# Kernel optimization log

Hardware: AMD Instinct MI355X
Metric: run time of the kernel (lower is better)

The kernel has to match this reference:

```python
import jax, jax.numpy as jnp
import numpy as np
from jax import lax

N_BOXES = 6000
IOU_THR = 0.5
CONF_THR = 0.6


def setup_inputs() -> dict:
    key = jax.random.key(0)
    k1, k2, k3 = jax.random.split(key, 3)
    # valid xyxy boxes: top-left in [0,1000), width/height in [1,101)
    xy = jax.random.uniform(k1, (N_BOXES, 2), dtype=jnp.float32) * 1000.0
    wh = jax.random.uniform(k2, (N_BOXES, 2), dtype=jnp.float32) * 100.0 + 1.0
    boxes = jnp.concatenate([xy, xy + wh], axis=-1)  # [N,4] x1,y1,x2,y2
    scores = jax.random.uniform(k3, (N_BOXES,), dtype=jnp.float32)
    return {"boxes": boxes, "scores": scores}


def _pairwise_iou(b):
    # b: [N,4] xyxy. Returns [N,N] IoU, coordinates handled separately to
    # avoid materializing [N,N,2] intermediates.
    x1, y1, x2, y2 = b[:, 0], b[:, 1], b[:, 2], b[:, 3]
    area = (x2 - x1) * (y2 - y1)  # [N]
    iw = jnp.clip(jnp.minimum(x2[:, None], x2[None, :]) - jnp.maximum(x1[:, None], x1[None, :]), 0.0)
    ih = jnp.clip(jnp.minimum(y2[:, None], y2[None, :]) - jnp.maximum(y1[:, None], y1[None, :]), 0.0)
    inter = iw * ih  # [N,N]
    return inter / (area[:, None] + area[None, :] - inter)


def reference(boxes, scores):
    """torchvision-style NMS (suppress IoU > 0.5) then confidence filter (>= 0.6).
    Returns masked scores [N]: score where the box survives both stages, else 0.
    (Fixed-shape mask form of the original index outputs, for jit compatibility.)
    """
    n = scores.shape[0]
    order = jnp.argsort(-scores)  # descending by confidence
    iou = _pairwise_iou(boxes[order])  # [N,N] in sorted order
    idx = jnp.arange(n)

    def body(suppressed, i):
        keep_i = jnp.logical_not(suppressed[i])
        # a kept box suppresses all lower-scoring boxes with IoU > threshold
        supp_new = keep_i & (iou[i] > IOU_THR) & (idx > i)
        return suppressed | supp_new, keep_i

    _, keep_sorted = lax.scan(body, jnp.zeros((n,), dtype=bool), idx)
    keep = jnp.zeros((n,), dtype=bool).at[order].set(keep_sorted)
    final = keep & (scores >= CONF_THR)
    return jnp.where(final, scores, 0.0)
```

## Files before the change

kernel.cpp:

```cpp
#include <hip/hip_runtime.h>
#include <stdint.h>

#define N_BOXES 6000
#define NT 94
#define NTP 96
#define NROWS (NTP * 64)
#define CAP 16
#define IOU_THR 0.5f
#define CONF_THR 0.6f

typedef unsigned long long u64;
typedef unsigned int u32;
typedef unsigned short u16;

#define BAR() asm volatile("s_waitcnt lgkmcnt(0)\n\ts_barrier" ::: "memory")

__device__ __forceinline__ u64 rdlane64(u64 v, int l) {
    unsigned lo = (unsigned)__builtin_amdgcn_readlane((int)(unsigned)v, l);
    unsigned hi = (unsigned)__builtin_amdgcn_readlane((int)(unsigned)(v >> 32), l);
    return ((u64)hi << 32) | lo;
}

__global__ void __launch_bounds__(1024) k_sort(const float* __restrict__ scores,
                                               const float4* __restrict__ boxes,
                                               int* __restrict__ sidx,
                                               float4* __restrict__ sboxes,
                                               u32* __restrict__ lists_w,
                                               int* __restrict__ cnt) {
    __shared__ u64 kt[N_BOXES];
    __shared__ int part[1024];
    const int tid = threadIdx.x;
    const int gtid = blockIdx.x * 1024 + tid;
    for (int j = gtid; j < NROWS * CAP / 2; j += NT * 1024) lists_w[j] = 0xFFFFFFFFu;
    for (int j = gtid; j < NROWS; j += NT * 1024) cnt[j] = 0;

    for (int j = tid; j < N_BOXES; j += 1024) {
        unsigned inv = ~__float_as_uint(scores[j]);
        kt[j] = ((u64)inv << 32) | (unsigned)j;
    }
    __syncthreads();
    const int il = tid & 63;
    const int i = blockIdx.x * 64 + il;
    const int j0 = (tid >> 6) * 375;
    u64 mykey = (i < N_BOXES) ? kt[i] : 0ull;
    int cntr = 0;
#pragma unroll 5
    for (int jj = 0; jj < 375; ++jj)
        cntr += (kt[j0 + jj] < mykey) ? 1 : 0;
    part[tid] = cntr;
    __syncthreads();
    if (tid < 64 && i < N_BOXES) {
        int r = 0;
#pragma unroll
        for (int s = 0; s < 16; ++s) r += part[il + 64 * s];
        sidx[r] = i;
        sboxes[r] = boxes[i];
    }
}

__global__ void k_mask(const float4* __restrict__ sboxes,
                       u16* __restrict__ lists, int* __restrict__ cnt,
                       u64* __restrict__ diagw) {
    int ct = blockIdx.x, rt = blockIdx.y;
    if (ct < rt) return;
    int lane = threadIdx.x;
    __shared__ float4 rb[64];
    int row0 = rt * 64;
    int rows = min(64, N_BOXES - row0);
    if (lane < rows) rb[lane] = sboxes[row0 + lane];
    __syncthreads();
    int j = ct * 64 + lane;
    bool jvalid = (j < N_BOXES);
    float4 cb = make_float4(0.f, 0.f, 1.f, 1.f);
    if (jvalid) cb = sboxes[j];
    float carea = (cb.z - cb.x) * (cb.w - cb.y);
    bool isdiag = (ct == rt);
    for (int i = 0; i < rows; ++i) {
        float4 rbx = rb[i];
        float rarea = (rbx.z - rbx.x) * (rbx.w - rbx.y);
        float iw = fmaxf(fminf(rbx.z, cb.z) - fmaxf(rbx.x, cb.x), 0.f);
        float ih = fmaxf(fminf(rbx.w, cb.w) - fmaxf(rbx.y, cb.y), 0.f);
        float inter = iw * ih;
        float iou = inter / ((rarea + carea) - inter);
        int row = row0 + i;
        bool pred = jvalid && (j > row) && (iou > IOU_THR);
        if (isdiag) {
            u64 bal = __ballot(pred);
            if (lane == (i & 63)) diagw[row] = bal;
        } else if (pred) {
            int slot = atomicAdd(&cnt[row], 1);
            if (slot < CAP) lists[row * CAP + slot] = (u16)j;
        }
    }
}

__global__ void __launch_bounds__(256) k_scan(const u16* __restrict__ lists,
                                              const u64* __restrict__ diagw,
                                              const int* __restrict__ sidx,
                                              const float* __restrict__ scores,
                                              float* __restrict__ out) {
    __shared__ u64 removed[NTP];
    __shared__ u64 kwbuf[NTP];
    const int tid   = threadIdx.x;
    const int lane  = tid & 63;
    const int row_l = tid >> 2;
    const int sg    = (tid & 3) * 4;
    if (tid < NTP) removed[tid] = 0;

    u64 L0, L1, L2, D0, D1, D2;
    L0 = *(const u64*)&lists[(0 * 64 + row_l) * CAP + sg];
    L1 = *(const u64*)&lists[(1 * 64 + row_l) * CAP + sg];
    L2 = *(const u64*)&lists[(2 * 64 + row_l) * CAP + sg];
    D0 = diagw[0 * 64 + lane];
    D1 = diagw[1 * 64 + lane];
    D2 = diagw[2 * 64 + lane];
    __syncthreads();

#define STEP(T, LUSE, DUSE)                                                    \
    {                                                                          \
        const u64 nz = __ballot(DUSE != 0ull);        \
        const int row0 = (T) * 64;                                             \
        const int rem = N_BOXES - row0;                                        \
        const u64 valid = (rem >= 64) ? ~0ull                                  \
                        : ((rem <= 0) ? 0ull : ((1ull << rem) - 1ull));        \
        u64 c = valid & ~removed[(T)];                                         \
        u64 kw = 0;                                                            \
        while (c) {                                                            \
            u64 blockers = c & nz;                                             \
            if (!blockers) { kw |= c; break; }             \
            int g = (int)__builtin_ctzll(blockers);                            \
            u64 below = c & ((1ull << g) - 1ull);         \
            kw |= below | (1ull << g);                                         \
            u64 df = rdlane64(DUSE, g);                     \
            c &= ~(df | below | (1ull << g));                                  \
        }                                                                      \
        if (tid == 0) kwbuf[(T)] = kw;                                         \
        if (((kw >> row_l) & 1ull) && LUSE != ~0ull) {                         \
            u16 e0 = (u16)(LUSE), e1 = (u16)(LUSE >> 16),                      \
                e2 = (u16)(LUSE >> 32), e3 = (u16)(LUSE >> 48);                \
            if (e0 != 0xFFFFu) atomicOr(&removed[e0 >> 6], 1ull << (e0 & 63)); \
            if (e1 != 0xFFFFu) atomicOr(&removed[e1 >> 6], 1ull << (e1 & 63)); \
            if (e2 != 0xFFFFu) atomicOr(&removed[e2 >> 6], 1ull << (e2 & 63)); \
            if (e3 != 0xFFFFu) atomicOr(&removed[e3 >> 6], 1ull << (e3 & 63)); \
        }                                                                      \
        const int tn = ((T) + 3 < NTP) ? ((T) + 3) : ((T) + 3 - NTP);          \
        LUSE = *(const u64*)&lists[(tn * 64 + row_l) * CAP + sg];              \
        DUSE = diagw[tn * 64 + lane];                                          \
        BAR();                                                                 \
    }

    for (int t = 0; t < NTP; t += 3) {
        STEP(t,     L0, D0)
        STEP(t + 1, L1, D1)
        STEP(t + 2, L2, D2)
    }
#undef STEP

    for (int p = tid; p < N_BOXES; p += 256) {
        int orig = sidx[p];
        float s = scores[orig];
        bool k = (kwbuf[p >> 6] >> (p & 63)) & 1ull;
        out[orig] = (k && (s >= CONF_THR)) ? s : 0.0f;
    }
}

extern "C" void kernel_launch(void* const* d_in, const int* in_sizes, int n_in,
                              void* d_out, int out_size, void* d_ws, size_t ws_size,
                              hipStream_t stream) {
    const float* boxes  = (const float*)d_in[0];
    const float* scores = (const float*)d_in[1];
    float* out = (float*)d_out;

    char* ws = (char*)d_ws;
    u16*    lists  = (u16*)(ws);
    int*    cnt    = (int*)(ws + 196608);
    u64*    diagw  = (u64*)(ws + 221184);
    int*    sidx   = (int*)(ws + 270336);
    float4* sboxes = (float4*)(ws + 294336);

    k_sort<<<dim3(NT), dim3(1024), 0, stream>>>(scores, (const float4*)boxes, sidx,
                                                sboxes, (u32*)lists, cnt);
    k_mask<<<dim3(NT, NT), dim3(64), 0, stream>>>((const float4*)sboxes, lists, cnt, diagw);
    k_scan<<<dim3(1), dim3(256), 0, stream>>>(lists, diagw, sidx, scores, out);
}
```

Measured before the change: 132.8 us.

## Run serial NMS scan in a single wavefront without block barriers, warm cache with other waves

The sequential tile scan now runs entirely in wave 0, with each lane handling a whole 16-entry suppression list. That removes the per-tile block-wide barrier, and the removed bitmask for the next tile is read after the wave's own LDS atomics. The other three waves stream the lists and diagonal buffers once and XOR the values into a dummy accumulator, which pulls them into cache for the latency-bound wave. The trade-off is more serial atomics per lane and reliance on in-wave ordering of LDS operations.

```diff
diff --git a/kernel.cpp b/kernel.cpp
--- a/kernel.cpp
+++ b/kernel.cpp
@@ -12,8 +12,6 @@
 typedef unsigned long long u64;
 typedef unsigned int u32;
 typedef unsigned short u16;
-
-#define BAR() asm volatile("s_waitcnt lgkmcnt(0)\n\ts_barrier" ::: "memory")
 
 __device__ __forceinline__ u64 rdlane64(u64 v, int l) {
     unsigned lo = (unsigned)__builtin_amdgcn_readlane((int)(unsigned)v, l);
@@ -101,60 +99,84 @@
                                               float* __restrict__ out) {
     __shared__ u64 removed[NTP];
     __shared__ u64 kwbuf[NTP];
-    const int tid   = threadIdx.x;
-    const int lane  = tid & 63;
-    const int row_l = tid >> 2;
-    const int sg    = (tid & 3) * 4;
+    const int tid = threadIdx.x;
     if (tid < NTP) removed[tid] = 0;
-
-    u64 L0, L1, L2, D0, D1, D2;
-    L0 = *(const u64*)&lists[(0 * 64 + row_l) * CAP + sg];
-    L1 = *(const u64*)&lists[(1 * 64 + row_l) * CAP + sg];
-    L2 = *(const u64*)&lists[(2 * 64 + row_l) * CAP + sg];
-    D0 = diagw[0 * 64 + lane];
-    D1 = diagw[1 * 64 + lane];
-    D2 = diagw[2 * 64 + lane];
-    __syncthreads();
-
-#define STEP(T, LUSE, DUSE)                                                    \
-    {                                                                          \
-        const u64 nz = __ballot(DUSE != 0ull);        \
-        const int row0 = (T) * 64;                                             \
-        const int rem = N_BOXES - row0;                                        \
-        const u64 valid = (rem >= 64) ? ~0ull                                  \
-                        : ((rem <= 0) ? 0ull : ((1ull << rem) - 1ull));        \
-        u64 c = valid & ~removed[(T)];                                         \
-        u64 kw = 0;                                                            \
-        while (c) {                                                            \
-            u64 blockers = c & nz;                                             \
-            if (!blockers) { kw |= c; break; }             \
-            int g = (int)__builtin_ctzll(blockers);                            \
-            u64 below = c & ((1ull << g) - 1ull);         \
-            kw |= below | (1ull << g);                                         \
-            u64 df = rdlane64(DUSE, g);                     \
-            c &= ~(df | below | (1ull << g));                                  \
-        }                                                                      \
-        if (tid == 0) kwbuf[(T)] = kw;                                         \
-        if (((kw >> row_l) & 1ull) && LUSE != ~0ull) {                         \
-            u16 e0 = (u16)(LUSE), e1 = (u16)(LUSE >> 16),                      \
-                e2 = (u16)(LUSE >> 32), e3 = (u16)(LUSE >> 48);                \
-            if (e0 != 0xFFFFu) atomicOr(&removed[e0 >> 6], 1ull << (e0 & 63)); \
+    __syncthreads();
+
+    if (tid >= 64) {
+        const uint4* lv = (const uint4*)lists;
+        const uint4* dv = (const uint4*)diagw;
+        u32 acc = 0;
+        for (int j = tid - 64; j < 12288; j += 192) {
+            uint4 v = lv[j];
+            acc ^= v.x ^ v.y ^ v.z ^ v.w;
+        }
+        for (int j = tid - 64; j < 3072; j += 192) {
+            uint4 v = dv[j];
+            acc ^= v.x ^ v.y ^ v.z ^ v.w;
+        }
+        asm volatile("" :: "v"(acc));
+    } else {
+        const int lane = tid;
+        uint4 A0 = *(const uint4*)&lists[(0 * 64 + lane) * CAP];
+        uint4 B0 = *(const uint4*)&lists[(0 * 64 + lane) * CAP + 8];
+        uint4 A1 = *(const uint4*)&lists[(1 * 64 + lane) * CAP];
+        uint4 B1 = *(const uint4*)&lists[(1 * 64 + lane) * CAP + 8];
+        uint4 A2 = *(const uint4*)&lists[(2 * 64 + lane) * CAP];
+        uint4 B2 = *(const uint4*)&lists[(2 * 64 + lane) * CAP + 8];
+        u64 D0 = diagw[0 * 64 + lane];
+        u64 D1 = diagw[1 * 64 + lane];
+        u64 D2 = diagw[2 * 64 + lane];
+        u64 rmn = 0;
+
+#define SC2(w)                                                                 \
+        if ((w) != 0xFFFFFFFFu) {                                              \
+            u16 e0 = (u16)(w), e1 = (u16)((w) >> 16);                          \
+            atomicOr(&removed[e0 >> 6], 1ull << (e0 & 63));                    \
             if (e1 != 0xFFFFu) atomicOr(&removed[e1 >> 6], 1ull << (e1 & 63)); \
-            if (e2 != 0xFFFFu) atomicOr(&removed[e2 >> 6], 1ull << (e2 & 63)); \
-            if (e3 != 0xFFFFu) atomicOr(&removed[e3 >> 6], 1ull << (e3 & 63)); \
-        }                                                                      \
-        const int tn = ((T) + 3 < NTP) ? ((T) + 3) : ((T) + 3 - NTP);          \
-        LUSE = *(const u64*)&lists[(tn * 64 + row_l) * CAP + sg];              \
-        DUSE = diagw[tn * 64 + lane];                                          \
-        BAR();                                                                 \
-    }
-
-    for (int t = 0; t < NTP; t += 3) {
-        STEP(t,     L0, D0)
-        STEP(t + 1, L1, D1)
-        STEP(t + 2, L2, D2)
-    }
+        }
+
+#define STEP(T, A, B, DD)                                                      \
+        {                                                                      \
+            const u64 nz = __ballot(DD != 0ull);      \
+            const int row0 = (T) * 64;                                         \
+            const int rem = N_BOXES - row0;                                    \
+            const u64 valid = (rem >= 64) ? ~0ull                              \
+                            : ((rem <= 0) ? 0ull : ((1ull << rem) - 1ull));    \
+            u64 c = valid & ~rmn;                                              \
+            u64 kw = 0;                                                        \
+            while (c) {                                                        \
+                u64 blockers = c & nz;                                         \
+                if (!blockers) { kw |= c; break; }         \
+                int g = (int)__builtin_ctzll(blockers);                        \
+                u64 below = c & ((1ull << g) - 1ull);     \
+                kw |= below | (1ull << g);                                     \
+                u64 df = rdlane64(DD, g);                   \
+                c &= ~(df | below | (1ull << g));                              \
+            }                                                                  \
+            if (((kw >> lane) & 1ull) && A.x != 0xFFFFFFFFu) {                 \
+                SC2(A.x) SC2(A.y) SC2(A.z) SC2(A.w)                            \
+                SC2(B.x) SC2(B.y) SC2(B.z) SC2(B.w)                            \
+            }                                                                  \
+              \
+               \
+            rmn = removed[((T) + 1 < NTP) ? (T) + 1 : 0];                      \
+            if (lane == 0) kwbuf[(T)] = kw;                                    \
+            const int tn = ((T) + 3 < NTP) ? ((T) + 3) : ((T) + 3 - NTP);      \
+            A = *(const uint4*)&lists[(tn * 64 + lane) * CAP];                 \
+            B = *(const uint4*)&lists[(tn * 64 + lane) * CAP + 8];             \
+            DD = diagw[tn * 64 + lane];                                        \
+        }
+
+        for (int t = 0; t < NTP; t += 3) {
+            STEP(t,     A0, B0, D0)
+            STEP(t + 1, A1, B1, D1)
+            STEP(t + 2, A2, B2, D2)
+        }
 #undef STEP
+#undef SC2
+    }
+    __syncthreads();
 
     for (int p = tid; p < N_BOXES; p += 256) {
         int orig = sidx[p];
```

After: 140.9 us. 6.1% more time.

## Use ballot-based rank sort and triangular grid for IoU mask kernel

Applied to the files above, without the earlier changes.

The rank sort no longer stages keys in shared memory with per-thread serial comparisons. Each wave now ranks four boxes by streaming all scores from global memory and counting smaller keys with ballot plus popcount. The mask kernel launches only the upper-triangular tile blocks, mapped from a linear block index, instead of a full square grid where half the blocks exit early. This cuts empty block launches and shared-memory sort overhead, at the cost of repeated global score reads per wave and a sqrt-based index decode.

```diff
diff --git a/kernel.cpp b/kernel.cpp
--- a/kernel.cpp
+++ b/kernel.cpp
@@ -6,6 +6,7 @@
 #define NTP 96
 #define NROWS (NTP * 64)
 #define CAP 16
+#define NCHUNK 94
 #define IOU_THR 0.5f
 #define CONF_THR 0.6f
 
@@ -27,42 +28,55 @@
                                                float4* __restrict__ sboxes,
                                                u32* __restrict__ lists_w,
                                                int* __restrict__ cnt) {
-    __shared__ u64 kt[N_BOXES];
-    __shared__ int part[1024];
     const int tid = threadIdx.x;
     const int gtid = blockIdx.x * 1024 + tid;
     for (int j = gtid; j < NROWS * CAP / 2; j += NT * 1024) lists_w[j] = 0xFFFFFFFFu;
     for (int j = gtid; j < NROWS; j += NT * 1024) cnt[j] = 0;
 
-    for (int j = tid; j < N_BOXES; j += 1024) {
-        unsigned inv = ~__float_as_uint(scores[j]);
-        kt[j] = ((u64)inv << 32) | (unsigned)j;
-    }
-    __syncthreads();
-    const int il = tid & 63;
-    const int i = blockIdx.x * 64 + il;
-    const int j0 = (tid >> 6) * 375;
-    u64 mykey = (i < N_BOXES) ? kt[i] : 0ull;
-    int cntr = 0;
-#pragma unroll 5
-    for (int jj = 0; jj < 375; ++jj)
-        cntr += (kt[j0 + jj] < mykey) ? 1 : 0;
-    part[tid] = cntr;
-    __syncthreads();
-    if (tid < 64 && i < N_BOXES) {
-        int r = 0;
+    const int w = tid >> 6;
+    const int lane = tid & 63;
+    u64 own[4];
+    int ob[4];
 #pragma unroll
-        for (int s = 0; s < 16; ++s) r += part[il + 64 * s];
-        sidx[r] = i;
-        sboxes[r] = boxes[i];
+    for (int q = 0; q < 4; ++q) {
+        ob[q] = blockIdx.x * 64 + w * 4 + q;
+        float s = (ob[q] < N_BOXES) ? scores[ob[q]] : 0.0f;
+        own[q] = ((u64)(~__float_as_uint(s)) << 32) | (unsigned)ob[q];
+    }
+    int rank0 = 0, rank1 = 0, rank2 = 0, rank3 = 0;
+#pragma unroll 2
+    for (int cb = 0; cb < NCHUNK; ++cb) {
+        int j = cb * 64 + lane;
+        u64 kk = ~0ull;
+        if (j < N_BOXES) {
+            unsigned inv = ~__float_as_uint(scores[j]);
+            kk = ((u64)inv << 32) | (unsigned)j;
+        }
+        rank0 += __popcll(__ballot(kk < own[0]));
+        rank1 += __popcll(__ballot(kk < own[1]));
+        rank2 += __popcll(__ballot(kk < own[2]));
+        rank3 += __popcll(__ballot(kk < own[3]));
+    }
+    if (lane == 0) {
+        int r[4] = {rank0, rank1, rank2, rank3};
+#pragma unroll
+        for (int q = 0; q < 4; ++q)
+            if (ob[q] < N_BOXES) {
+                sidx[r[q]] = ob[q];
+                sboxes[r[q]] = boxes[ob[q]];
+            }
     }
 }
 
 __global__ void k_mask(const float4* __restrict__ sboxes,
                        u16* __restrict__ lists, int* __restrict__ cnt,
                        u64* __restrict__ diagw) {
-    int ct = blockIdx.x, rt = blockIdx.y;
-    if (ct < rt) return;
+    const int b = blockIdx.x;
+    int v = (int)((sqrtf(8.0f * (float)b + 1.0f) - 1.0f) * 0.5f);
+    while ((v + 1) * (v + 2) / 2 <= b) ++v;
+    while (v * (v + 1) / 2 > b) --v;
+    const int rt = b - v * (v + 1) / 2;
+    const int ct = v;
     int lane = threadIdx.x;
     __shared__ float4 rb[64];
     int row0 = rt * 64;
@@ -180,6 +194,7 @@
 
     k_sort<<<dim3(NT), dim3(1024), 0, stream>>>(scores, (const float4*)boxes, sidx,
                                                 sboxes, (u32*)lists, cnt);
-    k_mask<<<dim3(NT, NT), dim3(64), 0, stream>>>((const float4*)sboxes, lists, cnt, diagw);
+    k_mask<<<dim3(NT * (NT + 1) / 2), dim3(64), 0, stream>>>((const float4*)sboxes,
+                                                             lists, cnt, diagw);
     k_scan<<<dim3(1), dim3(256), 0, stream>>>(lists, diagw, sidx, scores, out);
 }
```

Result: slower. 145.4 us (+9.4%).

## Fuse sort, mask and scan into one cooperative kernel with per-row-tile readiness flags

Applied to the files above, without the earlier changes.

Replaces the three launches with a single cooperative kernel. NT blocks sort, then after a grid sync compute the IoU mask over a flattened list of upper-triangle tile pairs. One extra block runs the sequential NMS scan, polling per-row-tile done counters so it can start on early tiles while the mask is still being computed. List entries switch to a zero-initialised, flag-bit encoding written with atomicOr so the scanner can read partially filled lists with atomic loads. This removes launch gaps and overlaps the serial scan with the mask work, at the cost of a grid sync, spin polling, and a fallback path if the cooperative launch fails.

```diff
diff --git a/kernel.cpp b/kernel.cpp
--- a/kernel.cpp
+++ b/kernel.cpp
@@ -1,11 +1,16 @@
 #include <hip/hip_runtime.h>
+#include <hip/hip_cooperative_groups.h>
 #include <stdint.h>
+
+namespace cg = cooperative_groups;
 
 #define N_BOXES 6000
 #define NT 94
 #define NTP 96
 #define NROWS (NTP * 64)
 #define CAP 16
+#define NPAIRS (NT * (NT + 1) / 2)
+#define NWAVES (NT * 16)
 #define IOU_THR 0.5f
 #define CONF_THR 0.6f
 
@@ -19,6 +24,192 @@
     unsigned lo = (unsigned)__builtin_amdgcn_readlane((int)(unsigned)v, l);
     unsigned hi = (unsigned)__builtin_amdgcn_readlane((int)(unsigned)(v >> 32), l);
     return ((u64)hi << 32) | lo;
+}
+
+__global__ void __launch_bounds__(1024) k_fused(
+        const float* __restrict__ scores, const float4* __restrict__ boxes,
+        int* __restrict__ sidx, float4* __restrict__ sboxes,
+        u16* __restrict__ lists, int* __restrict__ cnt,
+        u64* __restrict__ diagw, int* __restrict__ done,
+        float* __restrict__ out) {
+    __shared__ __align__(16) char shraw[52096];
+    u64*    kt      = (u64*)shraw;
+    int*    part    = (int*)(shraw + 48000);
+    float4* rb      = (float4*)shraw;
+    u64*    removed = (u64*)shraw;
+    u64*    kwbuf   = (u64*)(shraw + 768);
+
+    const int tid  = threadIdx.x;
+    const int bid  = blockIdx.x;
+    const int w    = tid >> 6;
+    const int lane = tid & 63;
+
+    if (bid < NT) {
+        const int gtid = bid * 1024 + tid;
+        u32* lists_w = (u32*)lists;
+        for (int j = gtid; j < NROWS * CAP / 2; j += NT * 1024) lists_w[j] = 0u;
+        for (int j = gtid; j < NROWS; j += NT * 1024) cnt[j] = 0;
+        for (int j = tid; j < N_BOXES; j += 1024) {
+            unsigned inv = ~__float_as_uint(scores[j]);
+            kt[j] = ((u64)inv << 32) | (unsigned)j;
+        }
+        __syncthreads();
+        const int i = bid * 64 + lane;
+        const int j0 = w * 375;
+        u64 mykey = (i < N_BOXES) ? kt[i] : 0ull;
+        int cntr = 0;
+#pragma unroll 5
+        for (int jj = 0; jj < 375; ++jj)
+            cntr += (kt[j0 + jj] < mykey) ? 1 : 0;
+        part[tid] = cntr;
+        __syncthreads();
+        if (tid < 64 && i < N_BOXES) {
+            int r = 0;
+#pragma unroll
+            for (int s = 0; s < 16; ++s) r += part[lane + 64 * s];
+            sidx[r] = i;
+            sboxes[r] = boxes[i];
+        }
+    } else {
+        if (tid < NTP) done[tid] = 0;
+    }
+    cg::this_grid().sync();
+
+    if (bid < NT) {
+        const int gw = bid * 16 + w;
+        u32* lw = (u32*)lists;
+        for (int p = gw; p < NPAIRS; p += NWAVES) {
+            int rt = (int)((189.0f - sqrtf(35721.0f - 8.0f * (float)p)) * 0.5f);
+            while ((189 * rt - rt * rt) / 2 > p) --rt;
+            while ((189 * (rt + 1) - (rt + 1) * (rt + 1)) / 2 <= p) ++rt;
+            const int ct = rt + (p - (189 * rt - rt * rt) / 2);
+            const int row0 = rt * 64;
+            const int rows = min(64, N_BOXES - row0);
+            if (lane < rows) rb[w * 64 + lane] = sboxes[row0 + lane];
+            const int j = ct * 64 + lane;
+            const bool jvalid = (j < N_BOXES);
+            float4 cb = make_float4(0.f, 0.f, 1.f, 1.f);
+            if (jvalid) cb = sboxes[j];
+            float carea = (cb.z - cb.x) * (cb.w - cb.y);
+            const bool isdiag = (ct == rt);
+            for (int i = 0; i < rows; ++i) {
+                float4 rbx = rb[w * 64 + i];
+                float rarea = (rbx.z - rbx.x) * (rbx.w - rbx.y);
+                float iw = fmaxf(fminf(rbx.z, cb.z) - fmaxf(rbx.x, cb.x), 0.f);
+                float ih = fmaxf(fminf(rbx.w, cb.w) - fmaxf(rbx.y, cb.y), 0.f);
+                float inter = iw * ih;
+                float iou = inter / ((rarea + carea) - inter);
+                int row = row0 + i;
+                bool pred = jvalid && (j > row) && (iou > IOU_THR);
+                if (isdiag) {
+                    u64 bal = __ballot(pred);
+                    if (lane == (i & 63))
+                        __hip_atomic_store(&diagw[row], bal, __ATOMIC_RELAXED,
+                                           __HIP_MEMORY_SCOPE_AGENT);
+                } else if (pred) {
+                    int slot = atomicAdd(&cnt[row], 1);
+                    if (slot < CAP) {
+                        int e = row * CAP + slot;
+                        u32 val = ((u32)j | 0x8000u) << ((e & 1) * 16);
+                        atomicOr(&lw[e >> 1], val);
+                    }
+                }
+            }
+            asm volatile("s_waitcnt vmcnt(0)" ::: "memory");
+            if (lane == 0)
+                __hip_atomic_fetch_add(&done[rt], 1, __ATOMIC_RELAXED,
+                                       __HIP_MEMORY_SCOPE_AGENT);
+        }
+        return;
+    }
+
+#define POLL()                                                                 \
+    {                                                                          \
+        bool r0_ = (__hip_atomic_load(&done[lane], __ATOMIC_RELAXED,           \
+                        __HIP_MEMORY_SCOPE_AGENT) == NT - lane);               \
+        int t1_ = 64 + lane;                                                   \
+        bool r1_ = (t1_ >= NT) || (__hip_atomic_load(&done[t1_],               \
+                        __ATOMIC_RELAXED, __HIP_MEMORY_SCOPE_AGENT)            \
+                        == NT - t1_);                                          \
+        u64 nb0_ = ~__ballot(r0_);                                             \
+        u64 nb1_ = ~__ballot(r1_);                                             \
+        rdy = nb0_ ? (int)__builtin_ctzll(nb0_)                                \
+                   : (nb1_ ? 64 + (int)__builtin_ctzll(nb1_) : 128);           \
+    }
+#define WAITR(need)                                                            \
+    while (rdy < (need)) { POLL(); if (rdy < (need)) __builtin_amdgcn_s_sleep(2); }
+#define ALD(p) __hip_atomic_load((u64*)(p), __ATOMIC_RELAXED, __HIP_MEMORY_SCOPE_AGENT)
+
+    if (tid < 256) {
+        const int row_l = tid >> 2;
+        const int sg    = (tid & 3) * 4;
+        if (tid < NTP) removed[tid] = 0;
+        int rdy = 0;
+        WAITR(3);
+        u64 L0, L1, L2, D0, D1, D2;
+        L0 = ALD(&lists[(0 * 64 + row_l) * CAP + sg]);
+        L1 = ALD(&lists[(1 * 64 + row_l) * CAP + sg]);
+        L2 = ALD(&lists[(2 * 64 + row_l) * CAP + sg]);
+        D0 = ALD(&diagw[0 * 64 + lane]);
+        D1 = ALD(&diagw[1 * 64 + lane]);
+        D2 = ALD(&diagw[2 * 64 + lane]);
+        __syncthreads();
+
+#define FSTEP(T, LUSE, DUSE)                                                   \
+    {                                                                          \
+        const u64 nz = __ballot(DUSE != 0ull);                                 \
+        const int row0 = (T) * 64;                                             \
+        const int rem = N_BOXES - row0;                                        \
+        const u64 valid = (rem >= 64) ? ~0ull                                  \
+                        : ((rem <= 0) ? 0ull : ((1ull << rem) - 1ull));        \
+        u64 c = valid & ~removed[(T)];                                         \
+        u64 kw = 0;                                                            \
+        while (c) {                                                            \
+            u64 blockers = c & nz;                                             \
+            if (!blockers) { kw |= c; break; }                                 \
+            int g = (int)__builtin_ctzll(blockers);                            \
+            u64 below = c & ((1ull << g) - 1ull);                              \
+            kw |= below | (1ull << g);                                         \
+            u64 df = rdlane64(DUSE, g);                                        \
+            c &= ~(df | below | (1ull << g));                                  \
+        }                                                                      \
+        if (tid == 0) kwbuf[(T)] = kw;                                         \
+        if (((kw >> row_l) & 1ull) && LUSE != 0ull) {                          \
+            u32 e0 = (u32)(LUSE) & 0xFFFFu, e1 = (u32)(LUSE) >> 16;            \
+            u32 e2 = (u32)(LUSE >> 32) & 0xFFFFu, e3 = (u32)(LUSE >> 48);      \
+            if (e0 & 0x8000u) atomicOr(&removed[(e0 & 0x7FFFu) >> 6], 1ull << (e0 & 63)); \
+            if (e1 & 0x8000u) atomicOr(&removed[(e1 & 0x7FFFu) >> 6], 1ull << (e1 & 63)); \
+            if (e2 & 0x8000u) atomicOr(&removed[(e2 & 0x7FFFu) >> 6], 1ull << (e2 & 63)); \
+            if (e3 & 0x8000u) atomicOr(&removed[(e3 & 0x7FFFu) >> 6], 1ull << (e3 & 63)); \
+        }                                                                      \
+        const int tn = ((T) + 3 < NTP) ? ((T) + 3) : ((T) + 3 - NTP);          \
+        const int nd = (tn < NT) ? tn + 1 : 0;                                 \
+        WAITR(nd);                                                             \
+        LUSE = ALD(&lists[(tn * 64 + row_l) * CAP + sg]);                      \
+        DUSE = ALD(&diagw[tn * 64 + lane]);                                    \
+        BAR();                                                                 \
+    }
+
+        for (int t = 0; t < NTP; t += 3) {
+            FSTEP(t,     L0, D0)
+            FSTEP(t + 1, L1, D1)
+            FSTEP(t + 2, L2, D2)
+        }
+#undef FSTEP
+    } else {
+        __syncthreads();
+        for (int t = 0; t < NTP; ++t) BAR();
+    }
+
+    for (int p = tid; p < N_BOXES; p += 1024) {
+        int orig = sidx[p];
+        float s = scores[orig];
+        bool k = (kwbuf[p >> 6] >> (p & 63)) & 1ull;
+        out[orig] = (k && (s >= CONF_THR)) ? s : 0.0f;
+    }
+#undef POLL
+#undef WAITR
+#undef ALD
 }
 
 __global__ void __launch_bounds__(1024) k_sort(const float* __restrict__ scores,
@@ -33,7 +224,6 @@
     const int gtid = blockIdx.x * 1024 + tid;
     for (int j = gtid; j < NROWS * CAP / 2; j += NT * 1024) lists_w[j] = 0xFFFFFFFFu;
     for (int j = gtid; j < NROWS; j += NT * 1024) cnt[j] = 0;
-
     for (int j = tid; j < N_BOXES; j += 1024) {
         unsigned inv = ~__float_as_uint(scores[j]);
         kt[j] = ((u64)inv << 32) | (unsigned)j;
@@ -106,7 +296,6 @@
     const int row_l = tid >> 2;
     const int sg    = (tid & 3) * 4;
     if (tid < NTP) removed[tid] = 0;
-
     u64 L0, L1, L2, D0, D1, D2;
     L0 = *(const u64*)&lists[(0 * 64 + row_l) * CAP + sg];
     L1 = *(const u64*)&lists[(1 * 64 + row_l) * CAP + sg];
@@ -115,10 +304,9 @@
     D1 = diagw[1 * 64 + lane];
     D2 = diagw[2 * 64 + lane];
     __syncthreads();
-
 #define STEP(T, LUSE, DUSE)                                                    \
     {                                                                          \
-        const u64 nz = __ballot(DUSE != 0ull);        \
+        const u64 nz = __ballot(DUSE != 0ull);                                 \
         const int row0 = (T) * 64;                                             \
         const int rem = N_BOXES - row0;                                        \
         const u64 valid = (rem >= 64) ? ~0ull                                  \
@@ -127,11 +315,11 @@
         u64 kw = 0;                                                            \
         while (c) {                                                            \
             u64 blockers = c & nz;                                             \
-            if (!blockers) { kw |= c; break; }             \
+            if (!blockers) { kw |= c; break; }                                 \
             int g = (int)__builtin_ctzll(blockers);                            \
-            u64 below = c & ((1ull << g) - 1ull);         \
+            u64 below = c & ((1ull << g) - 1ull);                              \
             kw |= below | (1ull << g);                                         \
-            u64 df = rdlane64(DUSE, g);                     \
+            u64 df = rdlane64(DUSE, g);                                        \
             c &= ~(df | below | (1ull << g));                                  \
         }                                                                      \
         if (tid == 0) kwbuf[(T)] = kw;                                         \
@@ -148,14 +336,12 @@
         DUSE = diagw[tn * 64 + lane];                                          \
         BAR();                                                                 \
     }
-
     for (int t = 0; t < NTP; t += 3) {
         STEP(t,     L0, D0)
         STEP(t + 1, L1, D1)
         STEP(t + 2, L2, D2)
     }
 #undef STEP
-
     for (int p = tid; p < N_BOXES; p += 256) {
         int orig = sidx[p];
         float s = scores[orig];
@@ -167,8 +353,8 @@
 extern "C" void kernel_launch(void* const* d_in, const int* in_sizes, int n_in,
                               void* d_out, int out_size, void* d_ws, size_t ws_size,
                               hipStream_t stream) {
-    const float* boxes  = (const float*)d_in[0];
-    const float* scores = (const float*)d_in[1];
+    const float4* boxes  = (const float4*)d_in[0];
+    const float*  scores = (const float*)d_in[1];
     float* out = (float*)d_out;
 
     char* ws = (char*)d_ws;
@@ -177,9 +363,18 @@
     u64*    diagw  = (u64*)(ws + 221184);
     int*    sidx   = (int*)(ws + 270336);
     float4* sboxes = (float4*)(ws + 294336);
-
-    k_sort<<<dim3(NT), dim3(1024), 0, stream>>>(scores, (const float4*)boxes, sidx,
-                                                sboxes, (u32*)lists, cnt);
-    k_mask<<<dim3(NT, NT), dim3(64), 0, stream>>>((const float4*)sboxes, lists, cnt, diagw);
-    k_scan<<<dim3(1), dim3(256), 0, stream>>>(lists, diagw, sidx, scores, out);
-}
+    int*    done   = (int*)(ws + 390336);
+
+    void* kargs[] = {(void*)&scores, (void*)&boxes, (void*)&sidx, (void*)&sboxes,
+                     (void*)&lists, (void*)&cnt, (void*)&diagw, (void*)&done,
+                     (void*)&out};
+    hipError_t e = hipLaunchCooperativeKernel(k_fused, dim3(NT + 1), dim3(1024),
+                                              kargs, 0u, stream);
+    if (e != hipSuccess) {
+        (void)hipGetLastError();
+        k_sort<<<dim3(NT), dim3(1024), 0, stream>>>(scores, boxes, sidx, sboxes,
+                                                    (u32*)lists, cnt);
+        k_mask<<<dim3(NT, NT), dim3(64), 0, stream>>>(sboxes, lists, cnt, diagw);
+        k_scan<<<dim3(1), dim3(256), 0, stream>>>(lists, diagw, sidx, scores, out);
+    }
+}
```

Measured after the change: 186.1 us. 1.4x slower.
